# Kernel optimization log

Measured on AMD Instinct MI355X. Metric: run time of the kernel, lower is better.

## Reference

```python
import jax, jax.numpy as jnp
import numpy as np

NUM_HEADS = 12

def setup_inputs() -> dict:
    key = jax.random.key(0)
    k1, k2, k3 = jax.random.split(key, 3)
    B, T, S, C = 8, 40, 1024, 768
    N = T + S
    x = jax.random.normal(k1, (B, N, C), dtype=jnp.float32)
    qkv_w = jax.random.normal(k2, (3 * C, C), dtype=jnp.float32) * (C ** -0.5)
    proj_w = jax.random.normal(k3, (C, C), dtype=jnp.float32) * (C ** -0.5)
    proj_b = jnp.zeros((C,), dtype=jnp.float32)
    return {"x": x, "qkv_w": qkv_w, "proj_w": proj_w, "proj_b": proj_b,
            "image_tokens": S, "text_tokens": T}


def reference(x, qkv_w, proj_w, proj_b, image_tokens, text_tokens):
    B, N, C = x.shape
    H = NUM_HEADS
    hd = C // H
    scale = hd ** -0.5
    # qkv: [B,N,3C] -> [3,B,H,N,hd]
    qkv = jnp.einsum('bnc,dc->bnd', x, qkv_w)
    qkv = qkv.reshape(B, N, 3, H, hd).transpose(2, 0, 3, 1, 4)
    q, k, v = qkv[0], qkv[1], qkv[2]
    # text block comes first in the token axis
    q_mt, q_s = q[:, :, :text_tokens], q[:, :, text_tokens:]
    k_mt = k[:, :, :text_tokens]
    v_mt = v[:, :, :text_tokens]
    # text -> text attention
    attn_mt = jax.nn.softmax(jnp.einsum('bhtd,bhsd->bhts', q_mt, k_mt) * scale, axis=-1)
    x_mt = jnp.einsum('bhts,bhsd->bhtd', attn_mt, v_mt)
    x_mt = x_mt.transpose(0, 2, 1, 3).reshape(B, text_tokens, C)
    # image -> all attention
    attn_s = jax.nn.softmax(jnp.einsum('bhid,bhnd->bhin', q_s, k) * scale, axis=-1)
    x_s = jnp.einsum('bhin,bhnd->bhid', attn_s, v)
    x_s = x_s.transpose(0, 2, 1, 3).reshape(B, image_tokens, C)
    out = jnp.concatenate([x_mt, x_s], axis=1)
    out = jnp.einsum('bnc,dc->bnd', out, proj_w) + proj_b
    return out
```

## Files before the change

kernel.cpp:

```cpp
#include <hip/hip_runtime.h>
#include <hip/hip_bf16.h>

typedef __bf16 bf16x8 __attribute__((ext_vector_type(8)));
typedef float f32x4 __attribute__((ext_vector_type(4)));

#define NHEADS 12
#define TT 40
#define ST 1024
#define NTOK 1064
#define CDIM 768
#define HD 64
#define QSCALE 0.18033688f

union U4 {
    uint4 u;
    __hip_bfloat16 h[8];
    bf16x8 v;
};

__device__ __forceinline__ void load_lds16(const __hip_bfloat16* g, __hip_bfloat16* s)
{
    __builtin_amdgcn_global_load_lds(
        (const __attribute__((address_space(1))) void*)g,
        (__attribute__((address_space(3))) void*)s, 16, 0, 0);
}

__global__ __launch_bounds__(256) void f2b3(
    const float* __restrict__ x,  __hip_bfloat16* __restrict__ xo,
    const float* __restrict__ w,  __hip_bfloat16* __restrict__ wo,
    const float* __restrict__ p,  __hip_bfloat16* __restrict__ po)
{
    const float* in; __hip_bfloat16* out; int i;
    if (blockIdx.x < 3192)      { in = x; out = xo; i = blockIdx.x * 256 + threadIdx.x; if (i >= 817152) return; }
    else if (blockIdx.x < 4056) { in = w; out = wo; i = (blockIdx.x - 3192) * 256 + threadIdx.x; if (i >= 221184) return; }
    else                        { in = p; out = po; i = (blockIdx.x - 4056) * 256 + threadIdx.x; if (i >= 73728) return; }
    float4 a = ((const float4*)in)[2 * i];
    float4 b = ((const float4*)in)[2 * i + 1];
    U4 r;
    r.h[0] = __float2bfloat16(a.x); r.h[1] = __float2bfloat16(a.y);
    r.h[2] = __float2bfloat16(a.z); r.h[3] = __float2bfloat16(a.w);
    r.h[4] = __float2bfloat16(b.x); r.h[5] = __float2bfloat16(b.y);
    r.h[6] = __float2bfloat16(b.z); r.h[7] = __float2bfloat16(b.w);
    ((uint4*)out)[i] = r.u;
}

template <int MODE>
__global__ __launch_bounds__(256) void gemm128(
    const __hip_bfloat16* __restrict__ A, int lda, int M,
    const __hip_bfloat16* __restrict__ B, int ldb,
    int K,
    __hip_bfloat16* __restrict__ out0,
    __hip_bfloat16* __restrict__ out1,
    __hip_bfloat16* __restrict__ out2,
    float* __restrict__ outf,
    const float* __restrict__ biasf)
{
    __shared__ __hip_bfloat16 lds[16384];

    const int tid = threadIdx.x;
    const int m0 = blockIdx.y * 128;
    const int n0 = blockIdx.x * 128;
    const int w = tid >> 6, l = tid & 63, l15 = l & 15, lq = l >> 4;
    const int wm = w >> 1, wn = w & 1;

    const __hip_bfloat16* srcA[2];
    const __hip_bfloat16* srcB[2];
    int c8[2];
#pragma unroll
    for (int rd = 0; rd < 2; ++rd) {
        const int c = tid + rd * 256;
        const int r = c >> 2, cs = c & 3;
        const int gs = (cs - (r >> 1)) & 3;
        int ra = m0 + r; if (ra > M - 1) ra = M - 1;
        srcA[rd] = A + (long long)ra * lda + gs * 8;
        srcB[rd] = B + (long long)(n0 + r) * ldb + gs * 8;
        c8[rd] = c * 8;
    }

    int offA[4], offB[4];
#pragma unroll
    for (int t = 0; t < 4; ++t) {
        { const int r = wm * 64 + t * 16 + l15;
          offA[t] = r * 32 + ((lq + (r >> 1)) & 3) * 8; }
        { const int r = wn * 64 + t * 16 + l15;
          offB[t] = r * 32 + ((lq + (r >> 1)) & 3) * 8; }
    }

    f32x4 acc[4][4] = {};

    const int ksteps = K / 32;
#pragma unroll
    for (int rd = 0; rd < 2; ++rd) {
        load_lds16(srcA[rd], lds + c8[rd]);
        load_lds16(srcB[rd], lds + 4096 + c8[rd]);
    }

    for (int ks = 0; ks < ksteps; ++ks) {
        __syncthreads();

        if (ks + 1 < ksteps) {
            const int o = ((ks + 1) & 1) * 8192;
            const int koff = (ks + 1) * 32;
#pragma unroll
            for (int rd = 0; rd < 2; ++rd) {
                load_lds16(srcA[rd] + koff, lds + o + c8[rd]);
                load_lds16(srcB[rd] + koff, lds + o + 4096 + c8[rd]);
            }
        }

        const __hip_bfloat16* bufA = lds + (ks & 1) * 8192;
        const __hip_bfloat16* bufB = bufA + 4096;

        bf16x8 af[4], bfr[4];
#pragma unroll
        for (int t = 0; t < 4; ++t) af[t] = *(const bf16x8*)(bufA + offA[t]);
#pragma unroll
        for (int t = 0; t < 4; ++t) bfr[t] = *(const bf16x8*)(bufB + offB[t]);
#pragma unroll
        for (int tr = 0; tr < 4; ++tr)
#pragma unroll
            for (int tc = 0; tc < 4; ++tc)
                acc[tr][tc] = __builtin_amdgcn_mfma_f32_16x16x32_bf16(af[tr], bfr[tc], acc[tr][tc], 0, 0, 0);
    }

    if (MODE == 0 && n0 >= 1536) {
        __hip_bfloat16* ldsT = lds;
#pragma unroll
        for (int hf = 0; hf < 2; ++hf) {
            __syncthreads();
            if (wn == hf) {
#pragma unroll
                for (int tr = 0; tr < 4; ++tr)
#pragma unroll
                    for (int tc = 0; tc < 4; ++tc) {
                        const int cl = tc * 16 + l15;
                        const int r = wm * 64 + tr * 16 + lq * 4;
                        U4 pk4;
                        pk4.h[0] = __float2bfloat16(acc[tr][tc][0]);
                        pk4.h[1] = __float2bfloat16(acc[tr][tc][1]);
                        pk4.h[2] = __float2bfloat16(acc[tr][tc][2]);
                        pk4.h[3] = __float2bfloat16(acc[tr][tc][3]);
                        *(uint2*)(ldsT + cl * 136 + r) = make_uint2(pk4.u.x, pk4.u.y);
                    }
            }
            __syncthreads();
            const int e = tid >> 2, rseg = (tid & 3) * 32;
            const int hh = (n0 + hf * 64 - 1536) >> 6;
#pragma unroll
            for (int j4 = 0; j4 < 4; ++j4) {
                const int r = rseg + j4 * 8;
                const int row = m0 + r;
                if (row >= 8 * NTOK) continue;
                const int b = row / NTOK;
                const int n = row - b * NTOK;
                __hip_bfloat16* dst = out2 + (((long long)(b * NHEADS + hh)) * HD + e) * NTOK + n;
                if (n + 8 <= NTOK) {
                    *(uint4*)dst = *(const uint4*)(ldsT + e * 136 + r);
                } else {
                    for (int j = 0; j < 8; ++j) {
                        const int row2 = row + j;
                        const int b2 = row2 / NTOK;
                        const int n2 = row2 - b2 * NTOK;
                        out2[(((long long)(b2 * NHEADS + hh)) * HD + e) * NTOK + n2] = ldsT[e * 136 + r + j];
                    }
                }
            }
        }
    } else {
#pragma unroll
        for (int tr = 0; tr < 4; ++tr) {
#pragma unroll
            for (int tc = 0; tc < 4; ++tc) {
                const int col = n0 + wn * 64 + tc * 16 + l15;
#pragma unroll
                for (int i = 0; i < 4; ++i) {
                    const int row = m0 + wm * 64 + tr * 16 + lq * 4 + i;
                    if (row >= M) continue;
                    const float v = acc[tr][tc][i];
                    if (MODE == 0) {
                        const int b = row / NTOK;
                        const int n = row - b * NTOK;
                        const int tq = col / CDIM;
                        const int rem = col - tq * CDIM;
                        const int h = rem >> 6;
                        const int e = rem & 63;
                        const long long gh = (long long)b * NHEADS + h;
                        if (tq == 0) out0[(gh * NTOK + n) * HD + e] = __float2bfloat16(v * QSCALE);
                        else         out1[(gh * NTOK + n) * HD + e] = __float2bfloat16(v);
                    } else {
                        outf[(long long)row * CDIM + col] = v + biasf[col];
                    }
                }
            }
        }
    }
}

__global__ __launch_bounds__(512) void flash_img(
    const __hip_bfloat16* __restrict__ Q,
    const __hip_bfloat16* __restrict__ Kt,
    const __hip_bfloat16* __restrict__ VT,
    __hip_bfloat16* __restrict__ AO)
{
    __shared__ __hip_bfloat16 smem[16384];
    const int gh = blockIdx.x;
    const int qt = blockIdx.y;
    const int tid = threadIdx.x;
    const int w = tid >> 6, l = tid & 63, l15 = l & 15, lq = l >> 4;

    const __hip_bfloat16* Kg = Kt + (long long)gh * NTOK * HD;
    const __hip_bfloat16* Vg = VT + (long long)gh * HD * NTOK;

    if (qt == 8) {
        const int b = gh / NHEADS;
        const int h = gh - b * NHEADS;
        float* fs = (float*)smem;
        float* Qs = fs;
        float* Ks = fs + 40 * 65;
        float* Vs = fs + 2 * 40 * 65;
        const __hip_bfloat16* Qg = Q + (long long)gh * NTOK * HD;
        for (int idx = tid; idx < 40 * 64; idx += 512) {
            const int n = idx >> 6;
            const int e = idx & 63;
            Qs[n * 65 + e] = __bfloat162float(Qg[n * HD + e]);
            Ks[n * 65 + e] = __bfloat162float(Kg[n * HD + e]);
            Vs[n * 65 + e] = __bfloat162float(Vg[(long long)e * NTOK + n]);
        }
        __syncthreads();
        for (int i = w; i < TT; i += 8) {
            float s = -1e30f;
            if (l < TT) {
                float a = 0.0f;
                for (int e = 0; e < 64; ++e) a += Qs[i * 65 + e] * Ks[l * 65 + e];
                s = a;
            }
            float m = s;
            for (int off = 32; off > 0; off >>= 1) m = fmaxf(m, __shfl_xor(m, off));
            float pr = (l < TT) ? exp2f(s - m) : 0.0f;
            float ssum = pr;
            for (int off = 32; off > 0; off >>= 1) ssum += __shfl_xor(ssum, off);
            pr /= ssum;
            float o = 0.0f;
            for (int j = 0; j < TT; ++j) o += __shfl(pr, j) * Vs[j * 65 + l];
            AO[((long long)b * NTOK + i) * CDIM + h * HD + l] = __float2bfloat16(o);
        }
        return;
    }

    const __hip_bfloat16* Qg = Q + ((long long)gh * NTOK + TT + qt * 128) * HD;

    const int r0 = tid >> 3;
    const int g0 = ((tid & 7) - r0) & 7;

    bf16x8 qf[2];
#pragma unroll
    for (int kk = 0; kk < 2; ++kk)
        qf[kk] = *(const bf16x8*)(Qg + (w * 16 + l15) * HD + kk * 32 + lq * 8);

    f32x4 ot[4] = {};
    float lsum = 0.0f;

    load_lds16(Kg + (long long)r0 * HD + g0 * 8, smem + tid * 8);
    load_lds16(Vg + (long long)r0 * NTOK + g0 * 8, smem + 4096 + tid * 8);

    const int segA = ((lq + l15) & 7) * 8;
    const int segB = ((4 + lq + l15) & 7) * 8;
    const int L0 = ((l & 16) ? 32 : 0) + l15;
    const int L1 = L0 + 16;
    const bool hi = (l & 32) != 0;

    for (int kt = 0; kt < 17; ++kt) {
        __syncthreads();

        if (kt < 16) {
            const int np = (kt + 1) * 64;
            __hip_bfloat16* kb = smem + ((kt + 1) & 1) * 8192;
            int kr = np + r0; if (kr > NTOK - 1) kr = NTOK - 1;
            int vc = np + g0 * 8; if (vc > NTOK - 8) vc = NTOK - 8;
            load_lds16(Kg + (long long)kr * HD + g0 * 8, kb + tid * 8);
            load_lds16(Vg + (long long)r0 * NTOK + vc, kb + 4096 + tid * 8);
        }

        const __hip_bfloat16* kbuf = smem + (kt & 1) * 8192;
        const __hip_bfloat16* vbuf = kbuf + 4096;

        f32x4 st[4] = {};
#pragma unroll
        for (int kk = 0; kk < 2; ++kk) {
            const int seg = kk ? segB : segA;
            bf16x8 kf[4];
#pragma unroll
            for (int t = 0; t < 4; ++t)
                kf[t] = *(const bf16x8*)(kbuf + (t * 16 + l15) * 64 + seg);
#pragma unroll
            for (int t = 0; t < 4; ++t)
                st[t] = __builtin_amdgcn_mfma_f32_16x16x32_bf16(kf[t], qf[kk], st[t], 0, 0, 0);
        }

        if (kt == 16) {
#pragma unroll
            for (int t = 0; t < 4; ++t) {
                const int nb = 1024 + t * 16 + lq * 4;
#pragma unroll
                for (int i = 0; i < 4; ++i)
                    if (nb + i >= NTOK) st[t][i] = -1e30f;
            }
        }

        float rs = 0.0f;
#pragma unroll
        for (int t = 0; t < 4; ++t)
#pragma unroll
            for (int i = 0; i < 4; ++i) {
                const float p = exp2f(st[t][i]);
                st[t][i] = p;
                rs += p;
            }
        lsum += rs;

        unsigned pk[4][2];
#pragma unroll
        for (int t = 0; t < 4; ++t)
#pragma unroll
            for (int h = 0; h < 2; ++h) {
                __hip_bfloat162 b2 = __float22bfloat162_rn(
                    make_float2(st[t][2 * h], st[t][2 * h + 1]));
                pk[t][h] = *(unsigned*)&b2;
            }

#pragma unroll
        for (int kk = 0; kk < 2; ++kk) {
            const int seg = kk ? segB : segA;
            bf16x8 vf[4];
#pragma unroll
            for (int te = 0; te < 4; ++te)
                vf[te] = *(const bf16x8*)(vbuf + (te * 16 + l15) * 64 + seg);
            const unsigned a0 = __shfl(pk[2 * kk][0], L0), b0 = __shfl(pk[2 * kk + 1][0], L0);
            const unsigned a1 = __shfl(pk[2 * kk][1], L0), b1 = __shfl(pk[2 * kk + 1][1], L0);
            const unsigned a2 = __shfl(pk[2 * kk][0], L1), b2 = __shfl(pk[2 * kk + 1][0], L1);
            const unsigned a3 = __shfl(pk[2 * kk][1], L1), b3 = __shfl(pk[2 * kk + 1][1], L1);
            union { unsigned u[4]; bf16x8 v; } pu;
            pu.u[0] = hi ? b0 : a0;
            pu.u[1] = hi ? b1 : a1;
            pu.u[2] = hi ? b2 : a2;
            pu.u[3] = hi ? b3 : a3;
#pragma unroll
            for (int te = 0; te < 4; ++te)
                ot[te] = __builtin_amdgcn_mfma_f32_16x16x32_bf16(vf[te], pu.v, ot[te], 0, 0, 0);
        }
    }

    lsum += __shfl_xor(lsum, 16);
    lsum += __shfl_xor(lsum, 32);

    __syncthreads();
    __hip_bfloat16* obuf = smem;
    const float inv = 1.0f / lsum;
#pragma unroll
    for (int te = 0; te < 4; ++te) {
        __hip_bfloat162 x0, x1;
        x0.x = __float2bfloat16(ot[te][0] * inv);
        x0.y = __float2bfloat16(ot[te][1] * inv);
        x1.x = __float2bfloat16(ot[te][2] * inv);
        x1.y = __float2bfloat16(ot[te][3] * inv);
        uint2 u;
        u.x = *(unsigned*)&x0;
        u.y = *(unsigned*)&x1;
        *(uint2*)(obuf + (w * 16 + l15) * 72 + te * 16 + lq * 4) = u;
    }
    __syncthreads();
    {
        const int b = gh / NHEADS, h = gh - b * NHEADS;
        const int r = tid >> 2, cc = (tid & 3) * 16;
        const int token = TT + qt * 128 + r;
        __hip_bfloat16* dst = AO + ((long long)b * NTOK + token) * CDIM + h * HD + cc;
        *(uint4*)dst       = *(const uint4*)(obuf + r * 72 + cc);
        *(uint4*)(dst + 8) = *(const uint4*)(obuf + r * 72 + cc + 8);
    }
}

extern "C" void kernel_launch(void* const* d_in, const int* in_sizes, int n_in,
                              void* d_out, int out_size, void* d_ws, size_t ws_size,
                              hipStream_t stream)
{
    const float* x      = (const float*)d_in[0];
    const float* qkv_w  = (const float*)d_in[1];
    const float* proj_w = (const float*)d_in[2];
    const float* proj_b = (const float*)d_in[3];
    float* out = (float*)d_out;

    const long long QKV_ELEMS = (long long)8 * NHEADS * NTOK * HD;
    __hip_bfloat16* Q  = (__hip_bfloat16*)d_ws;
    __hip_bfloat16* Kt = Q + QKV_ELEMS;
    __hip_bfloat16* VT = Kt + QKV_ELEMS;
    __hip_bfloat16* AO = VT + QKV_ELEMS;
    __hip_bfloat16* xb = AO;
    __hip_bfloat16* wb = AO + QKV_ELEMS;
    __hip_bfloat16* pb = wb + (long long)3 * CDIM * CDIM;

    f2b3<<<4344, 256, 0, stream>>>(x, xb, qkv_w, wb, proj_w, pb);

    gemm128<0><<<dim3(18, 67), 256, 0, stream>>>(
        xb, CDIM, 8 * NTOK, wb, CDIM, CDIM,
        Q, Kt, VT, nullptr, nullptr);

    flash_img<<<dim3(96, 9), 512, 0, stream>>>(Q, Kt, VT, AO);

    gemm128<3><<<dim3(6, 67), 256, 0, stream>>>(
        AO, CDIM, 8 * NTOK, pb, CDIM, CDIM,
        nullptr, nullptr, nullptr, out, proj_b);
}
```

Baseline: 219.7 us.

## Process 256 query rows per attention block to reuse K/V tiles

Each flash attention block now handles 256 image query rows, with two 16-row halves per wave, instead of 128. The grid drops from 9 to 5 tiles per head, so every K/V tile staged in LDS serves twice as many queries and global K/V traffic halves. The cost is more registers per thread for doubled accumulators and Q fragments (launch bounds now request 4 waves per EU), fewer blocks to fill the GPU, and a two-pass output staging through LDS.

```diff
diff --git a/kernel.cpp b/kernel.cpp
--- a/kernel.cpp
+++ b/kernel.cpp
@@ -196,7 +196,7 @@
     }
 }
 
-__global__ __launch_bounds__(512) void flash_img(
+__global__ __launch_bounds__(512, 4) void flash_img(
     const __hip_bfloat16* __restrict__ Q,
     const __hip_bfloat16* __restrict__ Kt,
     const __hip_bfloat16* __restrict__ VT,
@@ -211,7 +211,7 @@
     const __hip_bfloat16* Kg = Kt + (long long)gh * NTOK * HD;
     const __hip_bfloat16* Vg = VT + (long long)gh * HD * NTOK;
 
-    if (qt == 8) {
+    if (qt == 4) {
         const int b = gh / NHEADS;
         const int h = gh - b * NHEADS;
         float* fs = (float*)smem;
@@ -247,18 +247,20 @@
         return;
     }
 
-    const __hip_bfloat16* Qg = Q + ((long long)gh * NTOK + TT + qt * 128) * HD;
+    const __hip_bfloat16* Qg = Q + ((long long)gh * NTOK + TT + qt * 256) * HD;
 
     const int r0 = tid >> 3;
     const int g0 = ((tid & 7) - r0) & 7;
 
-    bf16x8 qf[2];
-#pragma unroll
-    for (int kk = 0; kk < 2; ++kk)
-        qf[kk] = *(const bf16x8*)(Qg + (w * 16 + l15) * HD + kk * 32 + lq * 8);
-
-    f32x4 ot[4] = {};
-    float lsum = 0.0f;
+    bf16x8 qf[2][2];
+#pragma unroll
+    for (int rh = 0; rh < 2; ++rh)
+#pragma unroll
+        for (int kk = 0; kk < 2; ++kk)
+            qf[rh][kk] = *(const bf16x8*)(Qg + (w * 32 + rh * 16 + l15) * HD + kk * 32 + lq * 8);
+
+    f32x4 ot[2][4] = {};
+    float lsum[2] = {0.0f, 0.0f};
 
     load_lds16(Kg + (long long)r0 * HD + g0 * 8, smem + tid * 8);
     load_lds16(Vg + (long long)r0 * NTOK + g0 * 8, smem + 4096 + tid * 8);
@@ -284,98 +286,114 @@
         const __hip_bfloat16* kbuf = smem + (kt & 1) * 8192;
         const __hip_bfloat16* vbuf = kbuf + 4096;
 
-        f32x4 st[4] = {};
-#pragma unroll
-        for (int kk = 0; kk < 2; ++kk) {
-            const int seg = kk ? segB : segA;
-            bf16x8 kf[4];
+#pragma unroll
+        for (int rh = 0; rh < 2; ++rh) {
+            f32x4 st[4] = {};
+#pragma unroll
+            for (int kk = 0; kk < 2; ++kk) {
+                const int seg = kk ? segB : segA;
+                bf16x8 kf[4];
+#pragma unroll
+                for (int t = 0; t < 4; ++t)
+                    kf[t] = *(const bf16x8*)(kbuf + (t * 16 + l15) * 64 + seg);
+#pragma unroll
+                for (int t = 0; t < 4; ++t)
+                    st[t] = __builtin_amdgcn_mfma_f32_16x16x32_bf16(kf[t], qf[rh][kk], st[t], 0, 0, 0);
+            }
+
+            if (kt == 16) {
+#pragma unroll
+                for (int t = 0; t < 4; ++t) {
+                    const int nb = 1024 + t * 16 + lq * 4;
+#pragma unroll
+                    for (int i = 0; i < 4; ++i)
+                        if (nb + i >= NTOK) st[t][i] = -1e30f;
+                }
+            }
+
+            float rs = 0.0f;
 #pragma unroll
             for (int t = 0; t < 4; ++t)
-                kf[t] = *(const bf16x8*)(kbuf + (t * 16 + l15) * 64 + seg);
+#pragma unroll
+                for (int i = 0; i < 4; ++i) {
+                    const float p = exp2f(st[t][i]);
+                    st[t][i] = p;
+                    rs += p;
+                }
+            lsum[rh] += rs;
+
+            unsigned pk[4][2];
 #pragma unroll
             for (int t = 0; t < 4; ++t)
-                st[t] = __builtin_amdgcn_mfma_f32_16x16x32_bf16(kf[t], qf[kk], st[t], 0, 0, 0);
-        }
-
-        if (kt == 16) {
-#pragma unroll
-            for (int t = 0; t < 4; ++t) {
-                const int nb = 1024 + t * 16 + lq * 4;
-#pragma unroll
-                for (int i = 0; i < 4; ++i)
-                    if (nb + i >= NTOK) st[t][i] = -1e30f;
-            }
-        }
-
-        float rs = 0.0f;
-#pragma unroll
-        for (int t = 0; t < 4; ++t)
-#pragma unroll
-            for (int i = 0; i < 4; ++i) {
-                const float p = exp2f(st[t][i]);
-                st[t][i] = p;
-                rs += p;
-            }
-        lsum += rs;
-
-        unsigned pk[4][2];
-#pragma unroll
-        for (int t = 0; t < 4; ++t)
-#pragma unroll
-            for (int h = 0; h < 2; ++h) {
-                __hip_bfloat162 b2 = __float22bfloat162_rn(
-                    make_float2(st[t][2 * h], st[t][2 * h + 1]));
-                pk[t][h] = *(unsigned*)&b2;
-            }
-
-#pragma unroll
-        for (int kk = 0; kk < 2; ++kk) {
-            const int seg = kk ? segB : segA;
-            bf16x8 vf[4];
-#pragma unroll
-            for (int te = 0; te < 4; ++te)
-                vf[te] = *(const bf16x8*)(vbuf + (te * 16 + l15) * 64 + seg);
-            const unsigned a0 = __shfl(pk[2 * kk][0], L0), b0 = __shfl(pk[2 * kk + 1][0], L0);
-            const unsigned a1 = __shfl(pk[2 * kk][1], L0), b1 = __shfl(pk[2 * kk + 1][1], L0);
-            const unsigned a2 = __shfl(pk[2 * kk][0], L1), b2 = __shfl(pk[2 * kk + 1][0], L1);
-            const unsigned a3 = __shfl(pk[2 * kk][1], L1), b3 = __shfl(pk[2 * kk + 1][1], L1);
-            union { unsigned u[4]; bf16x8 v; } pu;
-            pu.u[0] = hi ? b0 : a0;
-            pu.u[1] = hi ? b1 : a1;
-            pu.u[2] = hi ? b2 : a2;
-            pu.u[3] = hi ? b3 : a3;
-#pragma unroll
-            for (int te = 0; te < 4; ++te)
-                ot[te] = __builtin_amdgcn_mfma_f32_16x16x32_bf16(vf[te], pu.v, ot[te], 0, 0, 0);
-        }
-    }
-
-    lsum += __shfl_xor(lsum, 16);
-    lsum += __shfl_xor(lsum, 32);
-
-    __syncthreads();
+#pragma unroll
+                for (int h = 0; h < 2; ++h) {
+                    __hip_bfloat162 b2 = __float22bfloat162_rn(
+                        make_float2(st[t][2 * h], st[t][2 * h + 1]));
+                    pk[t][h] = *(unsigned*)&b2;
+                }
+
+#pragma unroll
+            for (int kk = 0; kk < 2; ++kk) {
+                const int seg = kk ? segB : segA;
+                bf16x8 vf[4];
+#pragma unroll
+                for (int te = 0; te < 4; ++te)
+                    vf[te] = *(const bf16x8*)(vbuf + (te * 16 + l15) * 64 + seg);
+                const unsigned a0 = __shfl(pk[2 * kk][0], L0), b0 = __shfl(pk[2 * kk + 1][0], L0);
+                const unsigned a1 = __shfl(pk[2 * kk][1], L0), b1 = __shfl(pk[2 * kk + 1][1], L0);
+                const unsigned a2 = __shfl(pk[2 * kk][0], L1), b2 = __shfl(pk[2 * kk + 1][0], L1);
+                const unsigned a3 = __shfl(pk[2 * kk][1], L1), b3 = __shfl(pk[2 * kk + 1][1], L1);
+                union { unsigned u[4]; bf16x8 v; } pu;
+                pu.u[0] = hi ? b0 : a0;
+                pu.u[1] = hi ? b1 : a1;
+                pu.u[2] = hi ? b2 : a2;
+                pu.u[3] = hi ? b3 : a3;
+#pragma unroll
+                for (int te = 0; te < 4; ++te)
+                    ot[rh][te] = __builtin_amdgcn_mfma_f32_16x16x32_bf16(vf[te], pu.v, ot[rh][te], 0, 0, 0);
+            }
+        }
+    }
+
+#pragma unroll
+    for (int rh = 0; rh < 2; ++rh) {
+        lsum[rh] += __shfl_xor(lsum[rh], 16);
+        lsum[rh] += __shfl_xor(lsum[rh], 32);
+    }
+    const float inv0 = 1.0f / lsum[0];
+    const float inv1 = 1.0f / lsum[1];
+
     __hip_bfloat16* obuf = smem;
-    const float inv = 1.0f / lsum;
-#pragma unroll
-    for (int te = 0; te < 4; ++te) {
-        __hip_bfloat162 x0, x1;
-        x0.x = __float2bfloat16(ot[te][0] * inv);
-        x0.y = __float2bfloat16(ot[te][1] * inv);
-        x1.x = __float2bfloat16(ot[te][2] * inv);
-        x1.y = __float2bfloat16(ot[te][3] * inv);
-        uint2 u;
-        u.x = *(unsigned*)&x0;
-        u.y = *(unsigned*)&x1;
-        *(uint2*)(obuf + (w * 16 + l15) * 72 + te * 16 + lq * 4) = u;
-    }
-    __syncthreads();
-    {
-        const int b = gh / NHEADS, h = gh - b * NHEADS;
-        const int r = tid >> 2, cc = (tid & 3) * 16;
-        const int token = TT + qt * 128 + r;
-        __hip_bfloat16* dst = AO + ((long long)b * NTOK + token) * CDIM + h * HD + cc;
-        *(uint4*)dst       = *(const uint4*)(obuf + r * 72 + cc);
-        *(uint4*)(dst + 8) = *(const uint4*)(obuf + r * 72 + cc + 8);
+    const int b = gh / NHEADS, h = gh - b * NHEADS;
+#pragma unroll
+    for (int p = 0; p < 2; ++p) {
+        __syncthreads();
+        if ((w >> 2) == p) {
+#pragma unroll
+            for (int rh = 0; rh < 2; ++rh) {
+                const float inv = rh ? inv1 : inv0;
+#pragma unroll
+                for (int te = 0; te < 4; ++te) {
+                    __hip_bfloat162 x0, x1;
+                    x0.x = __float2bfloat16(ot[rh][te][0] * inv);
+                    x0.y = __float2bfloat16(ot[rh][te][1] * inv);
+                    x1.x = __float2bfloat16(ot[rh][te][2] * inv);
+                    x1.y = __float2bfloat16(ot[rh][te][3] * inv);
+                    uint2 u;
+                    u.x = *(unsigned*)&x0;
+                    u.y = *(unsigned*)&x1;
+                    *(uint2*)(obuf + ((w & 3) * 32 + rh * 16 + l15) * 72 + te * 16 + lq * 4) = u;
+                }
+            }
+        }
+        __syncthreads();
+        {
+            const int r = tid >> 2, cc = (tid & 3) * 16;
+            const int token = TT + qt * 256 + p * 128 + r;
+            __hip_bfloat16* dst = AO + ((long long)b * NTOK + token) * CDIM + h * HD + cc;
+            *(uint4*)dst       = *(const uint4*)(obuf + r * 72 + cc);
+            *(uint4*)(dst + 8) = *(const uint4*)(obuf + r * 72 + cc + 8);
+        }
     }
 }
 
@@ -404,7 +422,7 @@
         xb, CDIM, 8 * NTOK, wb, CDIM, CDIM,
         Q, Kt, VT, nullptr, nullptr);
 
-    flash_img<<<dim3(96, 9), 512, 0, stream>>>(Q, Kt, VT, AO);
+    flash_img<<<dim3(96, 5), 512, 0, stream>>>(Q, Kt, VT, AO);
 
     gemm128<3><<<dim3(6, 67), 256, 0, stream>>>(
         AO, CDIM, 8 * NTOK, pb, CDIM, CDIM,
```

Result: slower. 224.2 us (+2.1%).
